# Kernel tuning notes

Measured on AMD Instinct MI355X. Metric: run time of the kernel, lower is better.

Reference implementation:

```python
import jax, jax.numpy as jnp
import numpy as np

B, N, D = 4, 2048, 1024
HEADS, DIM_HEAD = 16, 64
INNER = HEADS * DIM_HEAD  # 1024
SCALE = DIM_HEAD ** -0.5


def setup_inputs() -> dict:
    key = jax.random.key(0)
    ks = jax.random.split(key, 8)
    w = 0.02
    return {
        "x":  jax.random.normal(ks[0], (B, N, D), dtype=jnp.float32),
        "Wq": jax.random.normal(ks[1], (D, INNER), dtype=jnp.float32) * w,
        "bq": jax.random.normal(ks[2], (INNER,), dtype=jnp.float32) * w,
        "Wv": jax.random.normal(ks[3], (D, INNER), dtype=jnp.float32) * w,
        "bv": jax.random.normal(ks[4], (INNER,), dtype=jnp.float32) * w,
        "Wo": jax.random.normal(ks[5], (INNER, D), dtype=jnp.float32) * w,
        "bo": jax.random.normal(ks[6], (D,), dtype=jnp.float32) * w,
    }


def reference(x, Wq, bq, Wv, bv, Wo, bo):
    b, n, _ = x.shape
    q = x @ Wq + bq                      # [b, n, inner]
    v = x @ Wv + bv                      # [b, n, inner]
    # split heads -> [b, h, n, d]
    q = q.reshape(b, n, HEADS, DIM_HEAD).transpose(0, 2, 1, 3).astype(jnp.float32)
    v = v.reshape(b, n, HEADS, DIM_HEAD).transpose(0, 2, 1, 3)
    # k = q (self L2 attention)
    AB = jnp.einsum('bhid,bhjd->bhij', q, q)          # [b, h, n, n]
    AA = jnp.sum(q * q, axis=-1, keepdims=True)       # [b, h, n, 1]
    BB = jnp.swapaxes(AA, -1, -2)                     # [b, h, 1, n]
    sim = -(AA - 2.0 * AB + BB) * SCALE               # negative scaled L2 distance
    attn = jax.nn.softmax(sim, axis=-1)
    out = jnp.einsum('bhij,bhjd->bhid', attn, v)      # [b, h, n, d]
    out = out.transpose(0, 2, 1, 3).reshape(b, n, INNER)
    return out @ Wo + bo
```

## Files before the change

kernel.cpp:

```cpp
#include <hip/hip_runtime.h>
#include <hip/hip_bf16.h>

#define SEQ 2048
#define SCALE 0.125f
#define LOG2E 1.4426950408889634f
#define ALPHA 0.6005612049f

typedef __bf16 bf16;
typedef __bf16 bf16x4 __attribute__((ext_vector_type(4)));
typedef __bf16 bf16x8 __attribute__((ext_vector_type(8)));
typedef _Float16 f16;
typedef _Float16 f16x2 __attribute__((ext_vector_type(2)));
typedef _Float16 f16x4 __attribute__((ext_vector_type(4)));
typedef _Float16 f16x8 __attribute__((ext_vector_type(8)));
typedef float f32x4 __attribute__((ext_vector_type(4)));
typedef unsigned int u32;
typedef unsigned int u32x2 __attribute__((ext_vector_type(2)));
typedef unsigned int u32x4 __attribute__((ext_vector_type(4)));

__device__ __forceinline__ f16x2 pk_f16(float a, float b) {
    return __builtin_bit_cast(f16x2, __builtin_amdgcn_cvt_pkrtz(a, b));
}

__device__ __forceinline__ u32 pk_u32(float a, float b) {
    return __builtin_bit_cast(u32, __builtin_amdgcn_cvt_pkrtz(a, b));
}

__device__ __forceinline__ f32x4 mfma_f16_32(f16x8 a, f16x8 b, f32x4 c) {
    return __builtin_amdgcn_mfma_f32_16x16x32_f16(a, b, c, 0, 0, 0);
}

__device__ __forceinline__ void gl_lds16(const void* g, void* l) {
    __builtin_amdgcn_global_load_lds((const __attribute__((address_space(1))) u32*)g,
                                     (__attribute__((address_space(3))) u32*)l, 16, 0, 0);
}


__global__ __launch_bounds__(256) void k_cast_x(const float4* __restrict__ x,
                                                bf16x4* __restrict__ xb) {
    int t = blockIdx.x * 256 + threadIdx.x;
    float4 f = x[t];
    bf16x4 o;
    o[0] = (bf16)f.x; o[1] = (bf16)f.y; o[2] = (bf16)f.z; o[3] = (bf16)f.w;
    xb[t] = o;
}

__global__ __launch_bounds__(256) void k_transpose_cast(const float* __restrict__ src,
                                                        bf16* __restrict__ dst) {
    __shared__ float tile[32][33];
    int bx = blockIdx.x * 32;
    int by = blockIdx.y * 32;
    int tx = threadIdx.x;
    int ty = threadIdx.y;
#pragma unroll
    for (int j = 0; j < 32; j += 8)
        tile[ty + j][tx] = src[(size_t)(by + ty + j) * 1024 + bx + tx];
    __syncthreads();
#pragma unroll
    for (int j = 0; j < 32; j += 8)
        dst[(size_t)(bx + ty + j) * 1024 + by + tx] = (bf16)tile[tx][ty + j];
}


__global__ __launch_bounds__(256) void k_gemm_qv(const bf16* __restrict__ Xb,
                                                 const bf16* __restrict__ Wqvt,
                                                 const float* __restrict__ bq,
                                                 const float* __restrict__ bv,
                                                 bf16* __restrict__ Q,
                                                 f16* __restrict__ Vt,
                                                 float* __restrict__ QN) {
    constexpr int K = 1024;
    __shared__ bf16 As[128 * 32];
    __shared__ bf16 Bs[128 * 32];
    int t = threadIdx.x, w = t >> 6, l = t & 63;
    int blockN = blockIdx.x * 128, blockM = blockIdx.y * 128;
    int wm = w & 1, wn = w >> 1;
    int lr = l & 15, quad = l >> 4, q8 = quad * 8;
    int skcol = (l & 3) * 8;
    bool isQ = blockN < 1024;

    f32x4 acc[4][4] = {};
    const bf16* Ab = Xb + (size_t)blockM * K;
    const bf16* Bb = Wqvt + (size_t)blockN * K;

    for (int k0 = 0; k0 < K; k0 += 32) {
#pragma unroll
        for (int c2 = 0; c2 < 2; ++c2) {
            int c = 2 * w + c2;
            int row = c * 16 + (l >> 2);
            gl_lds16(Ab + (size_t)row * K + k0 + skcol, As + c * 512);
            gl_lds16(Bb + (size_t)row * K + k0 + skcol, Bs + c * 512);
        }
        __syncthreads();
        const bf16* Aw = As + wm * 64 * 32;
        const bf16* Bw = Bs + wn * 64 * 32;
        bf16x8 af[4], bfr[4];
#pragma unroll
        for (int mi = 0; mi < 4; ++mi) af[mi] = *(const bf16x8*)(Aw + (mi * 16 + lr) * 32 + q8);
#pragma unroll
        for (int ni = 0; ni < 4; ++ni) bfr[ni] = *(const bf16x8*)(Bw + (ni * 16 + lr) * 32 + q8);
        if (isQ) {
#pragma unroll
            for (int mi = 0; mi < 4; ++mi)
#pragma unroll
                for (int ni = 0; ni < 4; ++ni)
                    acc[mi][ni] = __builtin_amdgcn_mfma_f32_16x16x32_bf16(af[mi], bfr[ni], acc[mi][ni], 0, 0, 0);
        } else {
#pragma unroll
            for (int mi = 0; mi < 4; ++mi)
#pragma unroll
                for (int ni = 0; ni < 4; ++ni)
                    acc[mi][ni] = __builtin_amdgcn_mfma_f32_16x16x32_bf16(bfr[ni], af[mi], acc[mi][ni], 0, 0, 0);
        }
        __syncthreads();
    }

    int colbase = blockN + wn * 64;
    if (isQ) {
        int h = colbase >> 6;
        float bias[4];
#pragma unroll
        for (int ni = 0; ni < 4; ++ni) bias[ni] = bq[colbase + ni * 16 + lr];
#pragma unroll
        for (int mi = 0; mi < 4; ++mi) {
#pragma unroll
            for (int r = 0; r < 4; ++r) {
                int m = blockM + wm * 64 + mi * 16 + quad * 4 + r;
                int b = m >> 11, s = m & 2047;
                int bh = (b << 4) + h;
                float qsq = 0.f;
#pragma unroll
                for (int ni = 0; ni < 4; ++ni) {
                    float v = (acc[mi][ni][r] + bias[ni]) * ALPHA;
                    bf16 vb = (bf16)v;
                    Q[((size_t)bh * SEQ + s) * 64 + ni * 16 + lr] = vb;
                    float vr = (float)vb;
                    qsq += vr * vr;
                }
                qsq += __shfl_xor(qsq, 1);
                qsq += __shfl_xor(qsq, 2);
                qsq += __shfl_xor(qsq, 4);
                qsq += __shfl_xor(qsq, 8);
                if (lr == 0) QN[(size_t)bh * SEQ + s] = -0.5f * qsq;
            }
        }
    } else {
        int h = (colbase - 1024) >> 6;
        int b = blockM >> 11;
        int bh = (b << 4) + h;
        int s_base = (blockM & 2047) + wm * 64;
        const float* bvh = bv + (colbase - 1024);
#pragma unroll
        for (int ni = 0; ni < 4; ++ni) {
#pragma unroll
            for (int r = 0; r < 4; ++r) {
                int dh = ni * 16 + quad * 4 + r;
                float bias = bvh[dh];
#pragma unroll
                for (int mi = 0; mi < 4; ++mi) {
                    int s = s_base + mi * 16 + lr;
                    Vt[((size_t)bh * 64 + dh) * SEQ + s] = (f16)(acc[mi][ni][r] + bias);
                }
            }
        }
    }
}


__global__ __launch_bounds__(256, 4) void k_attn(const bf16* __restrict__ Q,
                                                 const f16* __restrict__ Vt,
                                                 const float* __restrict__ QN,
                                                 bf16* __restrict__ AO) {
    __shared__ bf16 Ks[64 * 64];
    __shared__ f16 Vs[64 * 64];
    __shared__ float BBl[2048];

    int t = threadIdx.x, w = t >> 6, l = t & 63;
    int bh = blockIdx.y;
    int i0 = blockIdx.x * 128;
    const bf16* Qh = Q + (size_t)bh * SEQ * 64;
    const f16* Vh = Vt + (size_t)bh * 64 * SEQ;
    int lr = l & 15, quad = l >> 4, q8 = quad * 8, lr7 = lr & 7;

    {
        const float4* QN4 = (const float4*)(QN + (size_t)bh * SEQ);
        float4* BB4 = (float4*)BBl;
        BB4[t] = QN4[t];
        BB4[t + 256] = QN4[t + 256];
    }

    bf16x8 af[2][2];
#pragma unroll
    for (int mi = 0; mi < 2; ++mi)
#pragma unroll
        for (int kc = 0; kc < 2; ++kc)
            af[mi][kc] = *(const bf16x8*)(Qh + (size_t)(i0 + w * 32 + mi * 16 + lr) * 64 + kc * 32 + q8);

    f32x4 oacc[2][4] = {};
    f32x4 dacc[2] = {};
    const f16x8 ones8 = {(f16)1.f, (f16)1.f, (f16)1.f, (f16)1.f,
                         (f16)1.f, (f16)1.f, (f16)1.f, (f16)1.f};

    int kb[2];
#pragma unroll
    for (int kc = 0; kc < 2; ++kc) kb[kc] = lr * 64 + (((kc * 4 + quad) ^ lr7) * 8);
    int voff[4];
#pragma unroll
    for (int di = 0; di < 4; ++di) voff[di] = (di * 16 + lr) * 64;
    int npo[2];
#pragma unroll
    for (int np = 0; np < 2; ++np) npo[np] = ((np * 4 + quad) ^ lr7) * 8;

    int sr0 = t >> 3, sc = t & 7;
    int sr1 = sr0 + 32;
    int sl0 = sr0 * 64 + ((sc ^ (sr0 & 7)) * 8);
    int sl1 = sr1 * 64 + ((sc ^ (sr1 & 7)) * 8);

    u32x4 rk0 = *(const u32x4*)(Qh + (size_t)sr0 * 64 + sc * 8);
    u32x4 rk1 = *(const u32x4*)(Qh + (size_t)sr1 * 64 + sc * 8);
    u32x4 rv0 = *(const u32x4*)(Vh + (size_t)sr0 * SEQ + sc * 8);
    u32x4 rv1 = *(const u32x4*)(Vh + (size_t)sr1 * SEQ + sc * 8);

    for (int j0 = 0; j0 < SEQ; j0 += 64) {
        __syncthreads();
        *(u32x4*)(Ks + sl0) = rk0;
        *(u32x4*)(Ks + sl1) = rk1;
        *(u32x4*)(Vs + sl0) = rv0;
        *(u32x4*)(Vs + sl1) = rv1;
        int jn = j0 + 64;
        if (jn < SEQ) {
            rk0 = *(const u32x4*)(Qh + (size_t)(jn + sr0) * 64 + sc * 8);
            rk1 = *(const u32x4*)(Qh + (size_t)(jn + sr1) * 64 + sc * 8);
            rv0 = *(const u32x4*)(Vh + (size_t)sr0 * SEQ + jn + sc * 8);
            rv1 = *(const u32x4*)(Vh + (size_t)sr1 * SEQ + jn + sc * 8);
        }
        __syncthreads();

#pragma unroll
        for (int np = 0; np < 2; ++np) {
            u32 hA[2][2], hB[2][2];
#pragma unroll
            for (int ni1 = 0; ni1 < 2; ++ni1) {
                int ni = np * 2 + ni1;
                bf16x8 bk0 = *(const bf16x8*)(Ks + ni * 1024 + kb[0]);
                bf16x8 bk1 = *(const bf16x8*)(Ks + ni * 1024 + kb[1]);
                f32x4 bbt = *(const f32x4*)(BBl + j0 + ni * 16 + quad * 4);
                f32x4 sT0 = bbt, sT1 = bbt;
                sT0 = __builtin_amdgcn_mfma_f32_16x16x32_bf16(bk0, af[0][0], sT0, 0, 0, 0);
                sT0 = __builtin_amdgcn_mfma_f32_16x16x32_bf16(bk1, af[0][1], sT0, 0, 0, 0);
                sT1 = __builtin_amdgcn_mfma_f32_16x16x32_bf16(bk0, af[1][0], sT1, 0, 0, 0);
                sT1 = __builtin_amdgcn_mfma_f32_16x16x32_bf16(bk1, af[1][1], sT1, 0, 0, 0);

                float p00 = __builtin_amdgcn_exp2f(sT0[0]);
                float p01 = __builtin_amdgcn_exp2f(sT0[1]);
                float p02 = __builtin_amdgcn_exp2f(sT0[2]);
                float p03 = __builtin_amdgcn_exp2f(sT0[3]);
                float p10 = __builtin_amdgcn_exp2f(sT1[0]);
                float p11 = __builtin_amdgcn_exp2f(sT1[1]);
                float p12 = __builtin_amdgcn_exp2f(sT1[2]);
                float p13 = __builtin_amdgcn_exp2f(sT1[3]);

                hA[ni1][0] = pk_u32(p00, p01);
                hA[ni1][1] = pk_u32(p02, p03);
                hB[ni1][0] = pk_u32(p10, p11);
                hB[ni1][1] = pk_u32(p12, p13);
            }
            f16x8 F8[2];
            {
                u32 a0 = hA[0][0], b0 = hA[1][0], a1 = hA[0][1], b1 = hA[1][1];
                asm("v_permlane32_swap_b32 %0, %1" : "+v"(a0), "+v"(b0));
                asm("v_permlane16_swap_b32 %0, %1" : "+v"(a0), "+v"(b0));
                asm("v_permlane32_swap_b32 %0, %1" : "+v"(a1), "+v"(b1));
                asm("v_permlane16_swap_b32 %0, %1" : "+v"(a1), "+v"(b1));
                u32x4 fu = {a0, a1, b0, b1};
                F8[0] = __builtin_bit_cast(f16x8, fu);
            }
            {
                u32 a0 = hB[0][0], b0 = hB[1][0], a1 = hB[0][1], b1 = hB[1][1];
                asm("v_permlane32_swap_b32 %0, %1" : "+v"(a0), "+v"(b0));
                asm("v_permlane16_swap_b32 %0, %1" : "+v"(a0), "+v"(b0));
                asm("v_permlane32_swap_b32 %0, %1" : "+v"(a1), "+v"(b1));
                asm("v_permlane16_swap_b32 %0, %1" : "+v"(a1), "+v"(b1));
                u32x4 fu = {a0, a1, b0, b1};
                F8[1] = __builtin_bit_cast(f16x8, fu);
            }

            dacc[0] = mfma_f16_32(F8[0], ones8, dacc[0]);
            dacc[1] = mfma_f16_32(F8[1], ones8, dacc[1]);

#pragma unroll
            for (int di = 0; di < 4; ++di) {
                f16x8 vf8 = *(const f16x8*)(Vs + voff[di] + npo[np]);
                oacc[0][di] = mfma_f16_32(F8[0], vf8, oacc[0][di]);
                oacc[1][di] = mfma_f16_32(F8[1], vf8, oacc[1][di]);
            }
        }
    }

    int b = bh >> 4, h = bh & 15;
#pragma unroll
    for (int mi = 0; mi < 2; ++mi) {
#pragma unroll
        for (int r = 0; r < 4; ++r) {
            float inv = 1.f / dacc[mi][r];
            int s = i0 + w * 32 + mi * 16 + quad * 4 + r;
#pragma unroll
            for (int di = 0; di < 4; ++di) {
                AO[((size_t)(b * SEQ + s)) * 1024 + h * 64 + di * 16 + lr] = (bf16)(oacc[mi][di][r] * inv);
            }
        }
    }
}


__global__ __launch_bounds__(256) void k_gemm_out(const bf16* __restrict__ AO,
                                                  const bf16* __restrict__ Wot,
                                                  const float* __restrict__ bo,
                                                  float* __restrict__ out) {
    constexpr int K = 1024;
    __shared__ bf16 As[128 * 32];
    __shared__ bf16 Bs[128 * 32];
    int t = threadIdx.x, w = t >> 6, l = t & 63;
    int blockN = blockIdx.x * 128, blockM = blockIdx.y * 128;
    int wm = w & 1, wn = w >> 1;
    int lr = l & 15, quad = l >> 4, q8 = quad * 8;
    int skcol = (l & 3) * 8;

    f32x4 acc[4][4] = {};
    const bf16* Ab = AO + (size_t)blockM * K;
    const bf16* Bb = Wot + (size_t)blockN * K;

    for (int k0 = 0; k0 < K; k0 += 32) {
#pragma unroll
        for (int c2 = 0; c2 < 2; ++c2) {
            int c = 2 * w + c2;
            int row = c * 16 + (l >> 2);
            gl_lds16(Ab + (size_t)row * K + k0 + skcol, As + c * 512);
            gl_lds16(Bb + (size_t)row * K + k0 + skcol, Bs + c * 512);
        }
        __syncthreads();
        const bf16* Aw = As + wm * 64 * 32;
        const bf16* Bw = Bs + wn * 64 * 32;
        bf16x8 af[4], bfr[4];
#pragma unroll
        for (int mi = 0; mi < 4; ++mi) af[mi] = *(const bf16x8*)(Aw + (mi * 16 + lr) * 32 + q8);
#pragma unroll
        for (int ni = 0; ni < 4; ++ni) bfr[ni] = *(const bf16x8*)(Bw + (ni * 16 + lr) * 32 + q8);
#pragma unroll
        for (int mi = 0; mi < 4; ++mi)
#pragma unroll
            for (int ni = 0; ni < 4; ++ni)
                acc[mi][ni] = __builtin_amdgcn_mfma_f32_16x16x32_bf16(af[mi], bfr[ni], acc[mi][ni], 0, 0, 0);
        __syncthreads();
    }

    int colbase = blockN + wn * 64;
    float bias[4];
#pragma unroll
    for (int ni = 0; ni < 4; ++ni) bias[ni] = bo[colbase + ni * 16 + lr];
#pragma unroll
    for (int mi = 0; mi < 4; ++mi) {
#pragma unroll
        for (int r = 0; r < 4; ++r) {
            int m = blockM + wm * 64 + mi * 16 + quad * 4 + r;
#pragma unroll
            for (int ni = 0; ni < 4; ++ni) {
                out[(size_t)m * 1024 + colbase + ni * 16 + lr] = acc[mi][ni][r] + bias[ni];
            }
        }
    }
}


extern "C" void kernel_launch(void* const* d_in, const int* in_sizes, int n_in,
                              void* d_out, int out_size, void* d_ws, size_t ws_size,
                              hipStream_t stream) {
    const float* x  = (const float*)d_in[0];
    const float* Wq = (const float*)d_in[1];
    const float* bq = (const float*)d_in[2];
    const float* Wv = (const float*)d_in[3];
    const float* bv = (const float*)d_in[4];
    const float* Wo = (const float*)d_in[5];
    const float* bo = (const float*)d_in[6];
    float* out = (float*)d_out;

    char* ws = (char*)d_ws;
    bf16* Xb   = (bf16*)ws;
    bf16* Wqvt = (bf16*)(ws + (size_t)(16 << 20));
    bf16* Wot  = (bf16*)(ws + (size_t)(20 << 20));
    bf16* Qb   = (bf16*)(ws + (size_t)(22 << 20));
    f16*  Vtb  = (f16*)(ws + (size_t)(38 << 20));
    float* QN  = (float*)(ws + (size_t)(54 << 20));
    bf16* AO   = Xb;

    k_cast_x<<<8192, 256, 0, stream>>>((const float4*)x, (bf16x4*)Xb);
    dim3 tb(32, 8);
    k_transpose_cast<<<dim3(32, 32), tb, 0, stream>>>(Wq, Wqvt);
    k_transpose_cast<<<dim3(32, 32), tb, 0, stream>>>(Wv, Wqvt + 1024 * 1024);
    k_transpose_cast<<<dim3(32, 32), tb, 0, stream>>>(Wo, Wot);
    k_gemm_qv<<<dim3(16, 64), 256, 0, stream>>>(Xb, Wqvt, bq, bv, Qb, Vtb, QN);
    k_attn<<<dim3(16, 64), 256, 0, stream>>>(Qb, Vtb, QN, AO);
    k_gemm_out<<<dim3(8, 64), 256, 0, stream>>>(AO, Wot, bo, out);
}
```

Baseline: 275.1 us.

## Shrink attention blocks to two waves, read row norms from global, add MFMA priority

```diff
diff --git a/kernel.cpp b/kernel.cpp
--- a/kernel.cpp
+++ b/kernel.cpp
@@ -167,27 +167,20 @@
 }
 
 
-__global__ __launch_bounds__(256, 4) void k_attn(const bf16* __restrict__ Q,
+__global__ __launch_bounds__(128, 4) void k_attn(const bf16* __restrict__ Q,
                                                  const f16* __restrict__ Vt,
                                                  const float* __restrict__ QN,
                                                  bf16* __restrict__ AO) {
     __shared__ bf16 Ks[64 * 64];
     __shared__ f16 Vs[64 * 64];
-    __shared__ float BBl[2048];
 
     int t = threadIdx.x, w = t >> 6, l = t & 63;
     int bh = blockIdx.y;
-    int i0 = blockIdx.x * 128;
+    int i0 = blockIdx.x * 64;
     const bf16* Qh = Q + (size_t)bh * SEQ * 64;
     const f16* Vh = Vt + (size_t)bh * 64 * SEQ;
+    const float* QNh = QN + (size_t)bh * SEQ;
     int lr = l & 15, quad = l >> 4, q8 = quad * 8, lr7 = lr & 7;
-
-    {
-        const float4* QN4 = (const float4*)(QN + (size_t)bh * SEQ);
-        float4* BB4 = (float4*)BBl;
-        BB4[t] = QN4[t];
-        BB4[t + 256] = QN4[t + 256];
-    }
 
     bf16x8 af[2][2];
 #pragma unroll
@@ -211,28 +204,35 @@
 #pragma unroll
     for (int np = 0; np < 2; ++np) npo[np] = ((np * 4 + quad) ^ lr7) * 8;
 
-    int sr0 = t >> 3, sc = t & 7;
-    int sr1 = sr0 + 32;
-    int sl0 = sr0 * 64 + ((sc ^ (sr0 & 7)) * 8);
-    int sl1 = sr1 * 64 + ((sc ^ (sr1 & 7)) * 8);
-
-    u32x4 rk0 = *(const u32x4*)(Qh + (size_t)sr0 * 64 + sc * 8);
-    u32x4 rk1 = *(const u32x4*)(Qh + (size_t)sr1 * 64 + sc * 8);
-    u32x4 rv0 = *(const u32x4*)(Vh + (size_t)sr0 * SEQ + sc * 8);
-    u32x4 rv1 = *(const u32x4*)(Vh + (size_t)sr1 * SEQ + sc * 8);
+    int sr = t >> 3, sc = t & 7;
+    int srr[4], sl[4];
+#pragma unroll
+    for (int i = 0; i < 4; ++i) {
+        srr[i] = sr + 16 * i;
+        sl[i] = srr[i] * 64 + ((sc ^ (srr[i] & 7)) * 8);
+    }
+
+    u32x4 rk[4], rv[4];
+#pragma unroll
+    for (int i = 0; i < 4; ++i) {
+        rk[i] = *(const u32x4*)(Qh + (size_t)srr[i] * 64 + sc * 8);
+        rv[i] = *(const u32x4*)(Vh + (size_t)srr[i] * SEQ + sc * 8);
+    }
 
     for (int j0 = 0; j0 < SEQ; j0 += 64) {
         __syncthreads();
-        *(u32x4*)(Ks + sl0) = rk0;
-        *(u32x4*)(Ks + sl1) = rk1;
-        *(u32x4*)(Vs + sl0) = rv0;
-        *(u32x4*)(Vs + sl1) = rv1;
+#pragma unroll
+        for (int i = 0; i < 4; ++i) {
+            *(u32x4*)(Ks + sl[i]) = rk[i];
+            *(u32x4*)(Vs + sl[i]) = rv[i];
+        }
         int jn = j0 + 64;
         if (jn < SEQ) {
-            rk0 = *(const u32x4*)(Qh + (size_t)(jn + sr0) * 64 + sc * 8);
-            rk1 = *(const u32x4*)(Qh + (size_t)(jn + sr1) * 64 + sc * 8);
-            rv0 = *(const u32x4*)(Vh + (size_t)sr0 * SEQ + jn + sc * 8);
-            rv1 = *(const u32x4*)(Vh + (size_t)sr1 * SEQ + jn + sc * 8);
+#pragma unroll
+            for (int i = 0; i < 4; ++i) {
+                rk[i] = *(const u32x4*)(Qh + (size_t)(jn + srr[i]) * 64 + sc * 8);
+                rv[i] = *(const u32x4*)(Vh + (size_t)srr[i] * SEQ + jn + sc * 8);
+            }
         }
         __syncthreads();
 
@@ -244,12 +244,14 @@
                 int ni = np * 2 + ni1;
                 bf16x8 bk0 = *(const bf16x8*)(Ks + ni * 1024 + kb[0]);
                 bf16x8 bk1 = *(const bf16x8*)(Ks + ni * 1024 + kb[1]);
-                f32x4 bbt = *(const f32x4*)(BBl + j0 + ni * 16 + quad * 4);
+                f32x4 bbt = *(const f32x4*)(QNh + j0 + ni * 16 + quad * 4);
                 f32x4 sT0 = bbt, sT1 = bbt;
+                __builtin_amdgcn_s_setprio(1);
                 sT0 = __builtin_amdgcn_mfma_f32_16x16x32_bf16(bk0, af[0][0], sT0, 0, 0, 0);
                 sT0 = __builtin_amdgcn_mfma_f32_16x16x32_bf16(bk1, af[0][1], sT0, 0, 0, 0);
                 sT1 = __builtin_amdgcn_mfma_f32_16x16x32_bf16(bk0, af[1][0], sT1, 0, 0, 0);
                 sT1 = __builtin_amdgcn_mfma_f32_16x16x32_bf16(bk1, af[1][1], sT1, 0, 0, 0);
+                __builtin_amdgcn_s_setprio(0);
 
                 float p00 = __builtin_amdgcn_exp2f(sT0[0]);
                 float p01 = __builtin_amdgcn_exp2f(sT0[1]);
@@ -285,6 +287,7 @@
                 F8[1] = __builtin_bit_cast(f16x8, fu);
             }
 
+            __builtin_amdgcn_s_setprio(1);
             dacc[0] = mfma_f16_32(F8[0], ones8, dacc[0]);
             dacc[1] = mfma_f16_32(F8[1], ones8, dacc[1]);
 
@@ -294,6 +297,7 @@
                 oacc[0][di] = mfma_f16_32(F8[0], vf8, oacc[0][di]);
                 oacc[1][di] = mfma_f16_32(F8[1], vf8, oacc[1][di]);
             }
+            __builtin_amdgcn_s_setprio(0);
         }
     }
 
@@ -399,6 +403,6 @@
     k_transpose_cast<<<dim3(32, 32), tb, 0, stream>>>(Wv, Wqvt + 1024 * 1024);
     k_transpose_cast<<<dim3(32, 32), tb, 0, stream>>>(Wo, Wot);
     k_gemm_qv<<<dim3(16, 64), 256, 0, stream>>>(Xb, Wqvt, bq, bv, Qb, Vtb, QN);
-    k_attn<<<dim3(16, 64), 256, 0, stream>>>(Qb, Vtb, QN, AO);
+    k_attn<<<dim3(32, 64), 128, 0, stream>>>(Qb, Vtb, QN, AO);
     k_gemm_out<<<dim3(8, 64), 256, 0, stream>>>(AO, Wot, bo, out);
 }
```

Result: slower. 313.0 us (+13.8%).
